# Kernel optimization log

Hardware: AMD Instinct MI355X
Metric: run time of the kernel (lower is better)

## Reference

```python
import jax, jax.numpy as jnp
import numpy as np

B, S, D, H = 2, 2048, 768, 12
HD = D // H


def setup_inputs() -> dict:
    key = jax.random.key(0)
    ks = jax.random.split(key, 8)
    scale = 1.0 / np.sqrt(D)
    inp = {
        "q": jax.random.normal(ks[0], (B, S, D), jnp.float32),
        "k": jax.random.normal(ks[1], (B, S, D), jnp.float32),
        "v": jax.random.normal(ks[2], (B, S, D), jnp.float32),
        # causal mask: 1.0 where attention is disallowed (upper triangle)
        "mask": jnp.triu(jnp.ones((S, S), jnp.float32), k=1)[None, None, :, :],
        "Wq": jax.random.normal(ks[3], (D, D), jnp.float32) * scale,
        "bq": jnp.zeros((D,), jnp.float32),
        "Wk": jax.random.normal(ks[4], (D, D), jnp.float32) * scale,
        "bk": jnp.zeros((D,), jnp.float32),
        "Wv": jax.random.normal(ks[5], (D, D), jnp.float32) * scale,
        "bv": jnp.zeros((D,), jnp.float32),
        "Wo": jax.random.normal(ks[6], (D, D), jnp.float32) * scale,
        "bo": jnp.zeros((D,), jnp.float32),
    }
    return inp


def _split_heads(x):
    # [B, S, D] -> [B, H, S, HD]
    b, s, _ = x.shape
    return x.reshape(b, s, H, HD).transpose(0, 2, 1, 3)


def reference(q, k, v, mask, Wq, bq, Wk, bk, Wv, bv, Wo, bo):
    qh = _split_heads(q @ Wq + bq)
    kh = _split_heads(k @ Wk + bk)
    vh = _split_heads(v @ Wv + bv)
    scale = 1.0 / jnp.sqrt(jnp.asarray(HD, qh.dtype))
    # [B, H, Sq, Sk] — full attention matrix, as in the original
    scores = jnp.einsum("bhqd,bhkd->bhqk", qh, kh) * scale
    scores = scores + mask * -1e9
    attn = jax.nn.softmax(scores, axis=-1)  # dropout is identity at inference
    out = jnp.einsum("bhqk,bhkd->bhqd", attn, vh)
    out = out.transpose(0, 2, 1, 3).reshape(q.shape[0], -1, D)
    return out @ Wo + bo
```

## Files before the change

### kernel.cpp

```cpp
#include <hip/hip_runtime.h>

#define SEQ    2048
#define NB     2
#define DMODEL 768
#define NH     12
#define HDIM   64
#define BS     (NB * SEQ)

typedef __bf16  bf16x8  __attribute__((ext_vector_type(8)));
typedef ushort  ushort8 __attribute__((ext_vector_type(8)));
typedef float   floatx4 __attribute__((ext_vector_type(4)));

#define GLOBAL_AS __attribute__((address_space(1)))
#define LDS_AS    __attribute__((address_space(3)))

union PackU8 { ushort u[8]; uint4 v; };

__device__ __forceinline__ ushort f2bf(float x) {
    union { float f; unsigned u; } t; t.f = x;
    unsigned r = t.u + 0x7fffu + ((t.u >> 16) & 1u);
    return (ushort)(r >> 16);
}

__device__ __forceinline__ unsigned bfpack(float hi, float lo) {
    union { float f; unsigned u; } a, b; a.f = hi; b.f = lo;
    return __builtin_amdgcn_perm(a.u, b.u, 0x07060302u);
}

__device__ __forceinline__ bf16x8 ld_frag(const ushort* p) {
    return __builtin_bit_cast(bf16x8, *(const ushort8*)p);
}

__global__ __launch_bounds__(256)
void convert_wT(const float* __restrict__ wq, const float* __restrict__ wk,
                const float* __restrict__ wv, const float* __restrict__ wo,
                ushort* __restrict__ wtcat, ushort* __restrict__ wto)
{
    __shared__ float Tf[64][69];
    const int z = blockIdx.z;
    const float* w = z == 0 ? wq : z == 1 ? wk : z == 2 ? wv : wo;
    ushort*      o = z < 3 ? wtcat + (size_t)z * DMODEL * DMODEL : wto;
    const int k0 = blockIdx.x * 64, n0 = blockIdx.y * 64;
    const int tid = threadIdx.x;
#pragma unroll
    for (int p = 0; p < 4; ++p) {
        const int idx = tid + p * 256;
        const int r = idx >> 4, c = (idx & 15) * 4;
        const float4 f = *(const float4*)&w[(size_t)(k0 + r) * DMODEL + n0 + c];
        Tf[r][c] = f.x; Tf[r][c + 1] = f.y; Tf[r][c + 2] = f.z; Tf[r][c + 3] = f.w;
    }
    __syncthreads();
#pragma unroll
    for (int p = 0; p < 2; ++p) {
        const int idx = tid + p * 256;
        const int n = idx >> 3, kk = (idx & 7) * 8;
        PackU8 pk;
#pragma unroll
        for (int j = 0; j < 8; ++j) pk.u[j] = f2bf(Tf[kk + j][n]);
        *(uint4*)&o[(size_t)(n0 + n) * DMODEL + k0 + kk] = pk.v;
    }
}

__global__ __launch_bounds__(256)
void gemm_qkv(const float* __restrict__ xq, const float* __restrict__ xk,
              const float* __restrict__ xv, const ushort* __restrict__ WT,
              const float* __restrict__ bq, const float* __restrict__ bk,
              const float* __restrict__ bv,
              ushort* __restrict__ oq, ushort* __restrict__ ok,
              ushort* __restrict__ ov)
{
    __shared__ __align__(16) ushort As[128 * 32];
    __shared__ __align__(16) ushort Bs[128 * 32];

    const int z = blockIdx.y / 6;
    const float* X = z == 0 ? xq : z == 1 ? xk : xv;

    const int tid  = threadIdx.x;
    const int lane = tid & 63;
    const int w    = tid >> 6;
    const int l15  = lane & 15;
    const int quad = lane >> 4;
    const int wm   = (w >> 1) * 64;
    const int wn   = (w & 1) * 64;
    const int row0 = blockIdx.x * 128;
    const int col0 = blockIdx.y * 128;

    floatx4 acc[4][4];
    const floatx4 fzero = {0.f, 0.f, 0.f, 0.f};
#pragma unroll
    for (int i = 0; i < 4; ++i)
#pragma unroll
        for (int j = 0; j < 4; ++j) acc[i][j] = fzero;

    const int rin = lane >> 2;
    const int gc  = (lane & 3) * 8;
    const int xr  = tid >> 1;
    const int xc  = (tid & 1) * 16;

    for (int k0 = 0; k0 < DMODEL; k0 += 32) {
#pragma unroll
        for (int p = 0; p < 2; ++p) {
            const int ch = w * 2 + p;
            const int r  = ch * 16 + rin;
            __builtin_amdgcn_global_load_lds(
                (const GLOBAL_AS uint*)&WT[(size_t)(col0 + r) * DMODEL + k0 + gc],
                (LDS_AS uint*)&Bs[ch * 512], 16, 0, 0);
        }
        {
            const float* Xr = X + (size_t)(row0 + xr) * DMODEL + k0 + xc;
            const float4 a0 = *(const float4*)(Xr);
            const float4 a1 = *(const float4*)(Xr + 4);
            const float4 a2 = *(const float4*)(Xr + 8);
            const float4 a3 = *(const float4*)(Xr + 12);
            uint4 w0, w1;
            w0.x = bfpack(a0.y, a0.x); w0.y = bfpack(a0.w, a0.z);
            w0.z = bfpack(a1.y, a1.x); w0.w = bfpack(a1.w, a1.z);
            w1.x = bfpack(a2.y, a2.x); w1.y = bfpack(a2.w, a2.z);
            w1.z = bfpack(a3.y, a3.x); w1.w = bfpack(a3.w, a3.z);
            *(uint4*)&As[xr * 32 + xc]     = w0;
            *(uint4*)&As[xr * 32 + xc + 8] = w1;
        }
        __syncthreads();

        bf16x8 af[4], bfr[4];
#pragma unroll
        for (int t = 0; t < 4; ++t) {
            af[t]  = ld_frag(&As[(wm + t * 16 + l15) * 32 + quad * 8]);
            bfr[t] = ld_frag(&Bs[(wn + t * 16 + l15) * 32 + quad * 8]);
        }
#pragma unroll
        for (int ti = 0; ti < 4; ++ti)
#pragma unroll
            for (int tj = 0; tj < 4; ++tj)
                acc[ti][tj] = __builtin_amdgcn_mfma_f32_16x16x32_bf16(
                    af[ti], bfr[tj], acc[ti][tj], 0, 0, 0);
        __syncthreads();
    }

    const int c0 = (blockIdx.y % 6) * 128;
    const float*  bias = z == 0 ? bq : z == 1 ? bk : bv;
    ushort*       out  = z == 0 ? oq : z == 1 ? ok : ov;
#pragma unroll
    for (int tj = 0; tj < 4; ++tj) {
        const int c_l = c0 + wn + tj * 16 + l15;
        const float bb = bias[c_l];
        const int h  = c_l >> 6;
        const int dd = c_l & 63;
#pragma unroll
        for (int ti = 0; ti < 4; ++ti) {
#pragma unroll
            for (int ri = 0; ri < 4; ++ri) {
                const int r_g = row0 + wm + ti * 16 + quad * 4 + ri;
                const int b   = r_g >> 11;
                const int s   = r_g & (SEQ - 1);
                out[(((size_t)(b * NH + h) * SEQ + s) << 6) + dd] =
                    f2bf(acc[ti][tj][ri] + bb);
            }
        }
    }
}

__global__ __launch_bounds__(256)
void gemm_out(const ushort* __restrict__ X, const ushort* __restrict__ WT,
              const float* __restrict__ bias, float* __restrict__ fo)
{
    __shared__ __align__(16) ushort As[64][40];
    __shared__ __align__(16) ushort Bs[128][40];

    const int tid  = threadIdx.x;
    const int lane = tid & 63;
    const int wv   = tid >> 6;
    const int wm   = (wv >> 1) * 32;
    const int wn   = (wv & 1) * 64;
    const int l15  = lane & 15;
    const int quad = lane >> 4;
    const int row0 = blockIdx.x * 64;
    const int col0 = blockIdx.y * 128;

    floatx4 acc[2][4];
    const floatx4 fzero = {0.f, 0.f, 0.f, 0.f};
#pragma unroll
    for (int i = 0; i < 2; ++i)
#pragma unroll
        for (int j = 0; j < 4; ++j) acc[i][j] = fzero;

    const int sr = tid >> 2;
    const int sc = (tid & 3) * 8;

    for (int k0 = 0; k0 < DMODEL; k0 += 32) {
        *(uint4*)&As[sr][sc] = *(const uint4*)&X[(size_t)(row0 + sr) * DMODEL + k0 + sc];
#pragma unroll
        for (int p = 0; p < 2; ++p) {
            const int r = sr + p * 64;
            *(uint4*)&Bs[r][sc] = *(const uint4*)&WT[(size_t)(col0 + r) * DMODEL + k0 + sc];
        }
        __syncthreads();

        bf16x8 af[2], bfr[4];
#pragma unroll
        for (int t = 0; t < 2; ++t)
            af[t] = ld_frag(&As[wm + t * 16 + l15][quad * 8]);
#pragma unroll
        for (int t = 0; t < 4; ++t)
            bfr[t] = ld_frag(&Bs[wn + t * 16 + l15][quad * 8]);
#pragma unroll
        for (int ti = 0; ti < 2; ++ti)
#pragma unroll
            for (int tj = 0; tj < 4; ++tj)
                acc[ti][tj] = __builtin_amdgcn_mfma_f32_16x16x32_bf16(
                    af[ti], bfr[tj], acc[ti][tj], 0, 0, 0);
        __syncthreads();
    }

#pragma unroll
    for (int tj = 0; tj < 4; ++tj) {
        const int c_g = col0 + wn + tj * 16 + l15;
        const float bb = bias[c_g];
#pragma unroll
        for (int ti = 0; ti < 2; ++ti)
#pragma unroll
            for (int ri = 0; ri < 4; ++ri) {
                const int r_g = row0 + wm + ti * 16 + quad * 4 + ri;
                fo[(size_t)r_g * DMODEL + c_g] = acc[ti][tj][ri] + bb;
            }
    }
}

__global__ void transpose_v(const ushort* __restrict__ vh, ushort* __restrict__ vt)
{
    __shared__ __align__(16) ushort T[64][72];
    const int bh = blockIdx.y;
    const int s0 = blockIdx.x * 64;
    const ushort* src = vh + (size_t)bh * SEQ * HDIM;
    ushort*       dst = vt + (size_t)bh * HDIM * SEQ;

#pragma unroll
    for (int p = 0; p < 2; ++p) {
        const int idx = threadIdx.x + p * 256;
        const int r = idx >> 3, c = (idx & 7) * 8;
        *(uint4*)&T[r][c] = *(const uint4*)&src[(size_t)(s0 + r) * HDIM + c];
    }
    __syncthreads();
#pragma unroll
    for (int p = 0; p < 2; ++p) {
        const int idx = threadIdx.x + p * 256;
        const int d = idx >> 3, c = (idx & 7) * 8;
        PackU8 pk;
#pragma unroll
        for (int j = 0; j < 8; ++j) pk.u[j] = T[c + j][d];
        *(uint4*)&dst[(size_t)d * SEQ + s0 + c] = pk.v;
    }
}

__global__ __launch_bounds__(128)
void attn_mfma(const ushort* __restrict__ qh, const ushort* __restrict__ kh,
               const ushort* __restrict__ vt, ushort* __restrict__ ctx)
{
    __shared__ __align__(16) ushort  Ps[2][32][32];
    __shared__ __align__(16) floatx4 OB[2][2][2][64];
    __shared__ float Lb[2][2][16];

    const int tid  = threadIdx.x;
    const int lane = tid & 63;
    const int w    = tid >> 6;
    const int l15  = lane & 15;
    const int quad = lane >> 4;
    const int id  = blockIdx.x;
    const int xcd = id & 7;
    const int jj  = id >> 3;
    const int g   = jj >> 5;
    const int x   = jj & 31;
    const int bh  = xcd + 8 * g;
    const int b   = bh / NH, h = bh - b * NH;
    const int qA  = x, qB = 63 - x;
    const int nkA = (qA >> 1) + 1;
    const size_t base = (size_t)bh * SEQ * HDIM;

    const float SCL = 0.125f * 1.44269504f;

    unsigned koff[2][2], voff[4];
#pragma unroll
    for (int nj = 0; nj < 2; ++nj)
#pragma unroll
        for (int ks = 0; ks < 2; ++ks)
            koff[nj][ks] = (unsigned)(w * 32 + nj * 16 + l15) * HDIM + ks * 32 + quad * 8;
#pragma unroll
    for (int dj = 0; dj < 4; ++dj)
        voff[dj] = (unsigned)(dj * 16 + l15) * SEQ + w * 32 + quad * 8;

    bf16x8 qf[2][2];
#pragma unroll
    for (int qt = 0; qt < 2; ++qt)
#pragma unroll
        for (int ks = 0; ks < 2; ++ks)
            qf[qt][ks] = ld_frag(&qh[base + (size_t)(qA * 32 + qt * 16 + l15) * HDIM
                                      + ks * 32 + quad * 8]);

    float lp[2] = {0.f, 0.f};
    floatx4 O[2][4];
    const floatx4 fzero = {0.f, 0.f, 0.f, 0.f};
#pragma unroll
    for (int mt = 0; mt < 2; ++mt)
#pragma unroll
        for (int dj = 0; dj < 4; ++dj) O[mt][dj] = fzero;

    auto epilogue = [&](int qtile) {
        float l0 = lp[0]; l0 += __shfl_xor(l0, 16); l0 += __shfl_xor(l0, 32);
        float l1 = lp[1]; l1 += __shfl_xor(l1, 16); l1 += __shfl_xor(l1, 32);
        if (quad == 0) { Lb[w][0][l15] = l0; Lb[w][1][l15] = l1; }
#pragma unroll
        for (int mt = 0; mt < 2; ++mt)
#pragma unroll
            for (int js = 0; js < 2; ++js)
                OB[w][mt][js][lane] = O[mt][w == 0 ? 2 + js : js];
        __syncthreads();
#pragma unroll
        for (int mt = 0; mt < 2; ++mt) {
            const floatx4 la = *(const floatx4*)&Lb[0][mt][quad * 4];
            const floatx4 lb = *(const floatx4*)&Lb[1][mt][quad * 4];
            floatx4 inv;
#pragma unroll
            for (int ri = 0; ri < 4; ++ri) inv[ri] = 1.f / (la[ri] + lb[ri]);
#pragma unroll
            for (int js = 0; js < 2; ++js) {
                const int dj = (w == 0) ? js : 2 + js;
                const floatx4 om = O[mt][dj] + OB[w ^ 1][mt][js][lane];
                const int col = h * HDIM + dj * 16 + l15;
#pragma unroll
                for (int ri = 0; ri < 4; ++ri) {
                    const int row = qtile * 32 + mt * 16 + quad * 4 + ri;
                    ctx[((size_t)b * SEQ + row) * DMODEL + col] = f2bf(om[ri] * inv[ri]);
                }
            }
        }
        __syncthreads();
    };

    for (int t = 0; t <= 32; ++t) {
        const bool isA = (t < nkA);
        const int  kt  = isA ? t : t - nkA;
        const int  c0  = kt * 64;
        const bool diag = (t == nkA - 1) || (t == 32);
        const int  qb0  = (isA ? qA : qB) * 32;
        const unsigned cK = (unsigned)c0 * HDIM;

        bf16x8 kf[2][2], vf[4];
#pragma unroll
        for (int nj = 0; nj < 2; ++nj)
#pragma unroll
            for (int ks = 0; ks < 2; ++ks)
                kf[nj][ks] = ld_frag(&kh[base + cK + koff[nj][ks]]);
#pragma unroll
        for (int dj = 0; dj < 4; ++dj)
            vf[dj] = ld_frag(&vt[base + (unsigned)c0 + voff[dj]]);

        floatx4 S[2][2];
#pragma unroll
        for (int nj = 0; nj < 2; ++nj)
#pragma unroll
            for (int qt = 0; qt < 2; ++qt) {
                S[nj][qt] = fzero;
#pragma unroll
                for (int ks = 0; ks < 2; ++ks)
                    S[nj][qt] = __builtin_amdgcn_mfma_f32_16x16x32_bf16(
                        kf[nj][ks], qf[qt][ks], S[nj][qt], 0, 0, 0);
            }

#pragma unroll
        for (int qt = 0; qt < 2; ++qt) {
            const int qrow = qb0 + qt * 16 + l15;
#pragma unroll
            for (int nj = 0; nj < 2; ++nj) {
                float p[4];
#pragma unroll
                for (int ri = 0; ri < 4; ++ri)
                    p[ri] = __builtin_amdgcn_exp2f(S[nj][qt][ri] * SCL);
                if (diag) {
#pragma unroll
                    for (int ri = 0; ri < 4; ++ri)
                        if (c0 + w * 32 + nj * 16 + quad * 4 + ri > qrow) p[ri] = 0.f;
                }
                lp[qt] += (p[0] + p[1]) + (p[2] + p[3]);
                uint2 pk;
                pk.x = bfpack(p[1], p[0]);
                pk.y = bfpack(p[3], p[2]);
                const int row    = qt * 16 + l15;
                const int chunkx = (nj * 2 + (quad >> 1)) ^ (l15 & 3);
                *(uint2*)&Ps[w][row][chunkx * 8 + (quad & 1) * 4] = pk;
            }
        }

        bf16x8 pf[2];
#pragma unroll
        for (int mt = 0; mt < 2; ++mt) {
            const int chunkx = quad ^ (l15 & 3);
            pf[mt] = ld_frag(&Ps[w][mt * 16 + l15][chunkx * 8]);
        }
#pragma unroll
        for (int mt = 0; mt < 2; ++mt)
#pragma unroll
            for (int dj = 0; dj < 4; ++dj)
                O[mt][dj] = __builtin_amdgcn_mfma_f32_16x16x32_bf16(
                    pf[mt], vf[dj], O[mt][dj], 0, 0, 0);

        if (t == nkA - 1) {
            epilogue(qA);
            lp[0] = lp[1] = 0.f;
#pragma unroll
            for (int mt = 0; mt < 2; ++mt)
#pragma unroll
                for (int dj = 0; dj < 4; ++dj) O[mt][dj] = fzero;
#pragma unroll
            for (int qt = 0; qt < 2; ++qt)
#pragma unroll
                for (int ks = 0; ks < 2; ++ks)
                    qf[qt][ks] = ld_frag(&qh[base + (size_t)(qB * 32 + qt * 16 + l15) * HDIM
                                              + ks * 32 + quad * 8]);
        }
    }

    epilogue(qB);
}

extern "C" void kernel_launch(void* const* d_in, const int* in_sizes, int n_in,
                              void* d_out, int out_size, void* d_ws, size_t ws_size,
                              hipStream_t stream)
{
    const float* q  = (const float*)d_in[0];
    const float* k  = (const float*)d_in[1];
    const float* v  = (const float*)d_in[2];
    const float* Wq = (const float*)d_in[4];
    const float* bq = (const float*)d_in[5];
    const float* Wk = (const float*)d_in[6];
    const float* bk = (const float*)d_in[7];
    const float* Wv = (const float*)d_in[8];
    const float* bv = (const float*)d_in[9];
    const float* Wo = (const float*)d_in[10];
    const float* bo = (const float*)d_in[11];
    float* out = (float*)d_out;

    char* ws = (char*)d_ws;
    const size_t ACT = (size_t)BS * DMODEL * 2;
    ushort* qhp   = (ushort*)(ws);
    ushort* khp   = (ushort*)(ws + ACT);
    ushort* vhp   = (ushort*)(ws + 2 * ACT);
    ushort* vhT   = (ushort*)(ws + 3 * ACT);
    ushort* ctx   = (ushort*)(ws + 4 * ACT);
    ushort* wtcat = (ushort*)(ws + 5 * ACT);
    ushort* wto   = wtcat + (size_t)3 * DMODEL * DMODEL;

    convert_wT<<<dim3(12, 12, 4), 256, 0, stream>>>(Wq, Wk, Wv, Wo, wtcat, wto);
    gemm_qkv<<<dim3(BS / 128, 18), 256, 0, stream>>>(
        q, k, v, wtcat, bq, bk, bv, qhp, khp, vhp);
    transpose_v<<<dim3(SEQ / 64, NB * NH), 256, 0, stream>>>(vhp, vhT);
    attn_mfma<<<dim3(768), 128, 0, stream>>>(qhp, khp, vhT, ctx);
    gemm_out<<<dim3(BS / 64, DMODEL / 128), 256, 0, stream>>>(ctx, wto, bo, out);
}
```

Before: 217.5 us.

## Split attention block into four waves and double-buffer K/V fragment loads

The attention kernel moves from 2 to 4 waves per block. Each wave now handles 16 query rows and half of each 64-key tile, which reduces per-wave MFMA and register work and raises wave-level parallelism. K and V fragments for the next tile are prefetched into a second register set while the current tile is computed, to hide global load latency. The price is more block-level synchronisation and an LDS reduction in the epilogue across the two key-split waves, plus extra register pressure from the doubled fragment buffers.

```diff
diff --git a/kernel.cpp b/kernel.cpp
--- a/kernel.cpp
+++ b/kernel.cpp
@@ -252,17 +252,19 @@
     }
 }
 
-__global__ __launch_bounds__(128)
+__global__ __launch_bounds__(256)
 void attn_mfma(const ushort* __restrict__ qh, const ushort* __restrict__ kh,
                const ushort* __restrict__ vt, ushort* __restrict__ ctx)
 {
-    __shared__ __align__(16) ushort  Ps[2][32][32];
-    __shared__ __align__(16) floatx4 OB[2][2][2][64];
-    __shared__ float Lb[2][2][16];
+    __shared__ __align__(16) ushort  Ps[4][16][32];
+    __shared__ __align__(16) floatx4 OB[2][4][64];
+    __shared__ float Lb[2][16];
 
     const int tid  = threadIdx.x;
     const int lane = tid & 63;
-    const int w    = tid >> 6;
+    const int wid  = tid >> 6;
+    const int w    = wid >> 1;
+    const int c    = wid & 1;
     const int l15  = lane & 15;
     const int quad = lane >> 4;
     const int id  = blockIdx.x;
@@ -277,149 +279,131 @@
     const size_t base = (size_t)bh * SEQ * HDIM;
 
     const float SCL = 0.125f * 1.44269504f;
-
-    unsigned koff[2][2], voff[4];
-#pragma unroll
-    for (int nj = 0; nj < 2; ++nj)
+    const int   sw  = (l15 >> 1) & 3;
+
+    bf16x8 qf[2];
+    auto load_q = [&](int qt) {
 #pragma unroll
         for (int ks = 0; ks < 2; ++ks)
-            koff[nj][ks] = (unsigned)(w * 32 + nj * 16 + l15) * HDIM + ks * 32 + quad * 8;
-#pragma unroll
-    for (int dj = 0; dj < 4; ++dj)
-        voff[dj] = (unsigned)(dj * 16 + l15) * SEQ + w * 32 + quad * 8;
-
-    bf16x8 qf[2][2];
-#pragma unroll
-    for (int qt = 0; qt < 2; ++qt)
-#pragma unroll
-        for (int ks = 0; ks < 2; ++ks)
-            qf[qt][ks] = ld_frag(&qh[base + (size_t)(qA * 32 + qt * 16 + l15) * HDIM
-                                      + ks * 32 + quad * 8]);
-
-    float lp[2] = {0.f, 0.f};
-    floatx4 O[2][4];
+            qf[ks] = ld_frag(&qh[base + (size_t)(qt * 32 + w * 16 + l15) * HDIM
+                                  + ks * 32 + quad * 8]);
+    };
+
+    auto load_kv = [&](int kt, bf16x8 (&kf)[2][2], bf16x8 (&vf)[4]) {
+        const int kc0 = kt * 64 + c * 32;
+#pragma unroll
+        for (int nj = 0; nj < 2; ++nj)
+#pragma unroll
+            for (int ks = 0; ks < 2; ++ks)
+                kf[nj][ks] = ld_frag(&kh[base + (size_t)(kc0 + nj * 16 + l15) * HDIM
+                                          + ks * 32 + quad * 8]);
+#pragma unroll
+        for (int dj = 0; dj < 4; ++dj)
+            vf[dj] = ld_frag(&vt[base + (size_t)(dj * 16 + l15) * SEQ + kc0 + quad * 8]);
+    };
+
+    float lp = 0.f;
+    floatx4 O[4];
     const floatx4 fzero = {0.f, 0.f, 0.f, 0.f};
 #pragma unroll
-    for (int mt = 0; mt < 2; ++mt)
-#pragma unroll
-        for (int dj = 0; dj < 4; ++dj) O[mt][dj] = fzero;
-
-    auto epilogue = [&](int qtile) {
-        float l0 = lp[0]; l0 += __shfl_xor(l0, 16); l0 += __shfl_xor(l0, 32);
-        float l1 = lp[1]; l1 += __shfl_xor(l1, 16); l1 += __shfl_xor(l1, 32);
-        if (quad == 0) { Lb[w][0][l15] = l0; Lb[w][1][l15] = l1; }
-#pragma unroll
-        for (int mt = 0; mt < 2; ++mt)
-#pragma unroll
-            for (int js = 0; js < 2; ++js)
-                OB[w][mt][js][lane] = O[mt][w == 0 ? 2 + js : js];
-        __syncthreads();
-#pragma unroll
-        for (int mt = 0; mt < 2; ++mt) {
-            const floatx4 la = *(const floatx4*)&Lb[0][mt][quad * 4];
-            const floatx4 lb = *(const floatx4*)&Lb[1][mt][quad * 4];
-            floatx4 inv;
-#pragma unroll
-            for (int ri = 0; ri < 4; ++ri) inv[ri] = 1.f / (la[ri] + lb[ri]);
-#pragma unroll
-            for (int js = 0; js < 2; ++js) {
-                const int dj = (w == 0) ? js : 2 + js;
-                const floatx4 om = O[mt][dj] + OB[w ^ 1][mt][js][lane];
-                const int col = h * HDIM + dj * 16 + l15;
-#pragma unroll
-                for (int ri = 0; ri < 4; ++ri) {
-                    const int row = qtile * 32 + mt * 16 + quad * 4 + ri;
-                    ctx[((size_t)b * SEQ + row) * DMODEL + col] = f2bf(om[ri] * inv[ri]);
+    for (int dj = 0; dj < 4; ++dj) O[dj] = fzero;
+
+    const int rowA = qA * 32 + w * 16 + l15;
+    const int rowB = qB * 32 + w * 16 + l15;
+
+    auto step = [&](int t, bf16x8 (&kf)[2][2], bf16x8 (&vf)[4],
+                    bf16x8 (&kfn)[2][2], bf16x8 (&vfn)[4]) {
+        if (t < 32) {
+            const int tn  = t + 1;
+            load_kv(tn < nkA ? tn : tn - nkA, kfn, vfn);
+        }
+        const bool isA  = (t < nkA);
+        const int  kt   = isA ? t : t - nkA;
+        const bool diag = (t == nkA - 1) || (t == 32);
+        const int  c0w  = kt * 64 + c * 32;
+        const int  qrow = isA ? rowA : rowB;
+
+        floatx4 S[2];
+#pragma unroll
+        for (int nj = 0; nj < 2; ++nj) {
+            S[nj] = fzero;
+#pragma unroll
+            for (int ks = 0; ks < 2; ++ks)
+                S[nj] = __builtin_amdgcn_mfma_f32_16x16x32_bf16(
+                    kf[nj][ks], qf[ks], S[nj], 0, 0, 0);
+        }
+
+#pragma unroll
+        for (int nj = 0; nj < 2; ++nj) {
+            float p[4];
+#pragma unroll
+            for (int ri = 0; ri < 4; ++ri)
+                p[ri] = __builtin_amdgcn_exp2f(S[nj][ri] * SCL);
+            if (diag) {
+#pragma unroll
+                for (int ri = 0; ri < 4; ++ri)
+                    if (c0w + nj * 16 + quad * 4 + ri > qrow) p[ri] = 0.f;
+            }
+            lp += (p[0] + p[1]) + (p[2] + p[3]);
+            uint2 pk;
+            pk.x = bfpack(p[1], p[0]);
+            pk.y = bfpack(p[3], p[2]);
+            const int c16 = (nj * 2 + (quad >> 1)) ^ sw;
+            *(uint2*)&Ps[wid][l15][c16 * 8 + (quad & 1) * 4] = pk;
+        }
+
+        const bf16x8 pf = ld_frag(&Ps[wid][l15][(quad ^ sw) * 8]);
+#pragma unroll
+        for (int dj = 0; dj < 4; ++dj)
+            O[dj] = __builtin_amdgcn_mfma_f32_16x16x32_bf16(pf, vf[dj], O[dj], 0, 0, 0);
+
+        if (diag) {
+            const int qt = isA ? qA : qB;
+            float lw = lp;
+            lw += __shfl_xor(lw, 16);
+            lw += __shfl_xor(lw, 32);
+            __syncthreads();
+            if (c == 1) {
+#pragma unroll
+                for (int dj = 0; dj < 4; ++dj) OB[w][dj][lane] = O[dj];
+                if (quad == 0) Lb[w][l15] = lw;
+            }
+            __syncthreads();
+            if (c == 0) {
+                const float inv = 1.f / (lw + Lb[w][l15]);
+                float ib[4];
+#pragma unroll
+                for (int ri = 0; ri < 4; ++ri) ib[ri] = __shfl(inv, quad * 4 + ri);
+#pragma unroll
+                for (int dj = 0; dj < 4; ++dj) {
+                    const floatx4 om = O[dj] + OB[w][dj][lane];
+                    const int col = h * HDIM + dj * 16 + l15;
+#pragma unroll
+                    for (int ri = 0; ri < 4; ++ri) {
+                        const int row = qt * 32 + w * 16 + quad * 4 + ri;
+                        ctx[((size_t)b * SEQ + row) * DMODEL + col] =
+                            f2bf(om[ri] * ib[ri]);
+                    }
                 }
             }
-        }
-        __syncthreads();
+            lp = 0.f;
+#pragma unroll
+            for (int dj = 0; dj < 4; ++dj) O[dj] = fzero;
+            if (t < 32) load_q(qB);
+        }
     };
 
-    for (int t = 0; t <= 32; ++t) {
-        const bool isA = (t < nkA);
-        const int  kt  = isA ? t : t - nkA;
-        const int  c0  = kt * 64;
-        const bool diag = (t == nkA - 1) || (t == 32);
-        const int  qb0  = (isA ? qA : qB) * 32;
-        const unsigned cK = (unsigned)c0 * HDIM;
-
-        bf16x8 kf[2][2], vf[4];
-#pragma unroll
-        for (int nj = 0; nj < 2; ++nj)
-#pragma unroll
-            for (int ks = 0; ks < 2; ++ks)
-                kf[nj][ks] = ld_frag(&kh[base + cK + koff[nj][ks]]);
-#pragma unroll
-        for (int dj = 0; dj < 4; ++dj)
-            vf[dj] = ld_frag(&vt[base + (unsigned)c0 + voff[dj]]);
-
-        floatx4 S[2][2];
-#pragma unroll
-        for (int nj = 0; nj < 2; ++nj)
-#pragma unroll
-            for (int qt = 0; qt < 2; ++qt) {
-                S[nj][qt] = fzero;
-#pragma unroll
-                for (int ks = 0; ks < 2; ++ks)
-                    S[nj][qt] = __builtin_amdgcn_mfma_f32_16x16x32_bf16(
-                        kf[nj][ks], qf[qt][ks], S[nj][qt], 0, 0, 0);
-            }
-
-#pragma unroll
-        for (int qt = 0; qt < 2; ++qt) {
-            const int qrow = qb0 + qt * 16 + l15;
-#pragma unroll
-            for (int nj = 0; nj < 2; ++nj) {
-                float p[4];
-#pragma unroll
-                for (int ri = 0; ri < 4; ++ri)
-                    p[ri] = __builtin_amdgcn_exp2f(S[nj][qt][ri] * SCL);
-                if (diag) {
-#pragma unroll
-                    for (int ri = 0; ri < 4; ++ri)
-                        if (c0 + w * 32 + nj * 16 + quad * 4 + ri > qrow) p[ri] = 0.f;
-                }
-                lp[qt] += (p[0] + p[1]) + (p[2] + p[3]);
-                uint2 pk;
-                pk.x = bfpack(p[1], p[0]);
-                pk.y = bfpack(p[3], p[2]);
-                const int row    = qt * 16 + l15;
-                const int chunkx = (nj * 2 + (quad >> 1)) ^ (l15 & 3);
-                *(uint2*)&Ps[w][row][chunkx * 8 + (quad & 1) * 4] = pk;
-            }
-        }
-
-        bf16x8 pf[2];
-#pragma unroll
-        for (int mt = 0; mt < 2; ++mt) {
-            const int chunkx = quad ^ (l15 & 3);
-            pf[mt] = ld_frag(&Ps[w][mt * 16 + l15][chunkx * 8]);
-        }
-#pragma unroll
-        for (int mt = 0; mt < 2; ++mt)
-#pragma unroll
-            for (int dj = 0; dj < 4; ++dj)
-                O[mt][dj] = __builtin_amdgcn_mfma_f32_16x16x32_bf16(
-                    pf[mt], vf[dj], O[mt][dj], 0, 0, 0);
-
-        if (t == nkA - 1) {
-            epilogue(qA);
-            lp[0] = lp[1] = 0.f;
-#pragma unroll
-            for (int mt = 0; mt < 2; ++mt)
-#pragma unroll
-                for (int dj = 0; dj < 4; ++dj) O[mt][dj] = fzero;
-#pragma unroll
-            for (int qt = 0; qt < 2; ++qt)
-#pragma unroll
-                for (int ks = 0; ks < 2; ++ks)
-                    qf[qt][ks] = ld_frag(&qh[base + (size_t)(qB * 32 + qt * 16 + l15) * HDIM
-                                              + ks * 32 + quad * 8]);
-        }
-    }
-
-    epilogue(qB);
+    bf16x8 k0[2][2], v0[4], k1[2][2], v1[4];
+    load_q(qA);
+    load_kv(0, k0, v0);
+
+    int t = 0;
+    while (true) {
+        step(t, k0, v0, k1, v1);
+        if (++t > 32) break;
+        step(t, k1, v1, k0, v0);
+        if (++t > 32) break;
+    }
 }
 
 extern "C" void kernel_launch(void* const* d_in, const int* in_sizes, int n_in,
@@ -453,6 +437,6 @@
     gemm_qkv<<<dim3(BS / 128, 18), 256, 0, stream>>>(
         q, k, v, wtcat, bq, bk, bv, qhp, khp, vhp);
     transpose_v<<<dim3(SEQ / 64, NB * NH), 256, 0, stream>>>(vhp, vhT);
-    attn_mfma<<<dim3(768), 128, 0, stream>>>(qhp, khp, vhT, ctx);
+    attn_mfma<<<dim3(768), 256, 0, stream>>>(qhp, khp, vhT, ctx);
     gemm_out<<<dim3(BS / 64, DMODEL / 128), 256, 0, stream>>>(ctx, wto, bo, out);
 }
```

After: 260.0 us. 1.2x slower.
